# Optimization experiments

Hardware: AMD Instinct MI355X
Metric: run time of the kernel (lower is better)

## Reference

```python
import jax, jax.numpy as jnp
import numpy as np

N_SRC = 20000
N_TGT = 20000
N_EDGE = 320000
D = 128            # in_dim == hid_dim
EDGE_IN = 2 * D + 1  # src feat + tgt feat + radial
COORD_MAX = 10.0


def _mlp2(x, w1, b1, w2, b2):
    # Linear -> SiLU -> Linear -> SiLU (edge MLP)
    h = jax.nn.silu(x @ w1 + b1)
    return jax.nn.silu(h @ w2 + b2)


def setup_inputs() -> dict:
    key = jax.random.key(0)
    ks = jax.random.split(key, 32)
    s = 0.05
    inp = {
        "src_node_feat": jax.random.normal(ks[0], (N_SRC, D), jnp.float32),
        "tgt_node_feat": jax.random.normal(ks[1], (N_TGT, D), jnp.float32),
        "src_node_coord": jax.random.normal(ks[2], (N_SRC, 3), jnp.float32),
        "tgt_node_coord": jax.random.normal(ks[3], (N_TGT, 3), jnp.float32),
        "edge_src": jax.random.randint(ks[4], (N_EDGE,), 0, N_SRC, jnp.int32),
        "edge_tgt": jax.random.randint(ks[5], (N_EDGE,), 0, N_TGT, jnp.int32),
        # edge MLP s2t
        "w1_s2t": jax.random.normal(ks[6], (EDGE_IN, D), jnp.float32) * s,
        "b1_s2t": jnp.zeros((D,), jnp.float32),
        "w2_s2t": jax.random.normal(ks[7], (D, D), jnp.float32) * s,
        "b2_s2t": jnp.zeros((D,), jnp.float32),
        # edge MLP t2s
        "w1_t2s": jax.random.normal(ks[8], (EDGE_IN, D), jnp.float32) * s,
        "b1_t2s": jnp.zeros((D,), jnp.float32),
        "w2_t2s": jax.random.normal(ks[9], (D, D), jnp.float32) * s,
        "b2_t2s": jnp.zeros((D,), jnp.float32),
        # gate MLPs (Linear(D,1) + Sigmoid)
        "wg_s2t": jax.random.normal(ks[10], (D, 1), jnp.float32) * s,
        "bg_s2t": jnp.zeros((1,), jnp.float32),
        "wg_t2s": jax.random.normal(ks[11], (D, 1), jnp.float32) * s,
        "bg_t2s": jnp.zeros((1,), jnp.float32),
        # coord MLP: Linear(D,D) + SiLU + Linear(D,1, bias=False, xavier gain 1e-3)
        "wc1": jax.random.normal(ks[12], (D, D), jnp.float32) * s,
        "bc1": jnp.zeros((D,), jnp.float32),
        "wc2": jax.random.normal(ks[13], (D, 1), jnp.float32) * 0.001,
        # node MLP tgt: Linear(2D,D) + SiLU + Linear(D,D)
        "wn1_t": jax.random.normal(ks[14], (2 * D, D), jnp.float32) * s,
        "bn1_t": jnp.zeros((D,), jnp.float32),
        "wn2_t": jax.random.normal(ks[15], (D, D), jnp.float32) * s,
        "bn2_t": jnp.zeros((D,), jnp.float32),
        # node MLP src
        "wn1_s": jax.random.normal(ks[16], (2 * D, D), jnp.float32) * s,
        "bn1_s": jnp.zeros((D,), jnp.float32),
        "wn2_s": jax.random.normal(ks[17], (D, D), jnp.float32) * s,
        "bn2_s": jnp.zeros((D,), jnp.float32),
    }
    return inp


def reference(src_node_feat, tgt_node_feat, src_node_coord, tgt_node_coord,
              edge_src, edge_tgt,
              w1_s2t, b1_s2t, w2_s2t, b2_s2t,
              w1_t2s, b1_t2s, w2_t2s, b2_t2s,
              wg_s2t, bg_s2t, wg_t2s, bg_t2s,
              wc1, bc1, wc2,
              wn1_t, bn1_t, wn2_t, bn2_t,
              wn1_s, bn1_s, wn2_s, bn2_s):
    # ---- coord2radial ----
    coord_diff = tgt_node_coord[edge_tgt] - src_node_coord[edge_src]  # [E,3]
    radial = jnp.sum(coord_diff ** 2, axis=1, keepdims=True)          # [E,1]

    # ---- edge function (gather + concat + two edge MLPs + gates) ----
    edge_in = jnp.concatenate(
        [src_node_feat[edge_src], tgt_node_feat[edge_tgt], radial], axis=1)  # [E, 257]
    e_s2t = _mlp2(edge_in, w1_s2t, b1_s2t, w2_s2t, b2_s2t)  # [E,D]
    e_t2s = _mlp2(edge_in, w1_t2s, b1_t2s, w2_t2s, b2_t2s)  # [E,D]
    e_s2t = e_s2t * jax.nn.sigmoid(e_s2t @ wg_s2t + bg_s2t)
    e_t2s = e_t2s * jax.nn.sigmoid(e_t2s @ wg_t2s + bg_t2s)

    # ---- coord update (coords_agg='mean', output_coord=True) ----
    coord_w = jax.nn.silu(e_s2t @ wc1 + bc1) @ wc2          # [E,1]
    weighted_trans = coord_diff * coord_w                   # [E,3]
    trans_sum = jax.ops.segment_sum(weighted_trans, edge_tgt, num_segments=N_TGT)
    cnt = jax.ops.segment_sum(jnp.ones((weighted_trans.shape[0],), jnp.float32),
                              edge_tgt, num_segments=N_TGT)
    agg_trans = trans_sum / jnp.maximum(cnt, 1.0)[:, None]
    tgt_coord_out = tgt_node_coord + jnp.clip(agg_trans, -COORD_MAX, COORD_MAX)

    # ---- node function (scatter-add aggregation + node MLPs + residual) ----
    agg_s2t = jax.ops.segment_sum(e_s2t, edge_tgt, num_segments=N_TGT)  # [Nt,D]
    agg_t2s = jax.ops.segment_sum(e_t2s, edge_src, num_segments=N_SRC)  # [Ns,D]
    tgt_in = jnp.concatenate([tgt_node_feat, agg_s2t], axis=1)  # [Nt,2D]
    src_in = jnp.concatenate([src_node_feat, agg_t2s], axis=1)  # [Ns,2D]
    tgt_out = jax.nn.silu(tgt_in @ wn1_t + bn1_t) @ wn2_t + bn2_t
    src_out = jax.nn.silu(src_in @ wn1_s + bn1_s) @ wn2_s + bn2_s
    tgt_out = tgt_node_feat + tgt_out  # residual (dims match)
    src_out = src_node_feat + src_out

    return src_out, tgt_out, src_node_coord, tgt_coord_out
```

## Files before the change

kernel.cpp:

```cpp
#include <hip/hip_runtime.h>

#define NN 20000
#define NEDGE 320000
#define COORD_MAX 10.0f

#define LDH 136
#define TILE_N 64
#define LDN  264

typedef __attribute__((ext_vector_type(4))) float f32x4;
typedef __attribute__((ext_vector_type(8))) short short8;
typedef __attribute__((ext_vector_type(8))) __bf16 bf16x8;

static __device__ __forceinline__ f32x4 mfma16(short8 a, short8 b, f32x4 c) {
  return __builtin_amdgcn_mfma_f32_16x16x32_bf16(
      __builtin_bit_cast(bf16x8, a), __builtin_bit_cast(bf16x8, b), c, 0, 0, 0);
}
static __device__ __forceinline__ unsigned short f2bf(float f) {
  unsigned u = __builtin_bit_cast(unsigned, f);
  u += 0x7FFFu + ((u >> 16) & 1u);
  return (unsigned short)(u >> 16);
}
static __device__ __forceinline__ float bf2f(unsigned short u) {
  unsigned x = ((unsigned)u) << 16;
  return __builtin_bit_cast(float, x);
}
static __device__ __forceinline__ unsigned cvtpk(float lo, float hi) {
  unsigned r;
  asm("v_cvt_pk_bf16_f32 %0, %1, %2" : "=v"(r) : "v"(lo), "v"(hi));
  return r;
}
static __device__ __forceinline__ float sigm(float x) {
  return __builtin_amdgcn_rcpf(1.f + __expf(-x));
}
static __device__ __forceinline__ float silu_(float x) { return x * sigm(x); }

struct PackJobs {
  const float* w[11];
  unsigned short* o[11];
  int kreal[11];
  int nk[11];
};

__global__ void egnn_prep(PackJobs J,
                          const int* __restrict__ eTgt, const int* __restrict__ eSrc,
                          int* __restrict__ cntT, int* __restrict__ cntS,
                          float* __restrict__ aggZero ) {
  const int job = blockIdx.y;
  const int idx = blockIdx.x * 256 + threadIdx.x;
  if (job < 11) {
    const int nk = J.nk[job];
    if (idx >= nk * 512) return;
    const float* w = J.w[job];
    const int kreal = J.kreal[job];
    const int lane = idx & 63;
    const int ct = (idx >> 6) & 7;
    const int kstep = idx >> 9;
    const int col = ct * 16 + (lane & 15);
    const int k0 = kstep * 32 + (lane >> 4) * 8;
    union { short8 s; unsigned short u[8]; } t;
#pragma unroll
    for (int j = 0; j < 8; ++j) {
      int k = k0 + j;
      t.u[j] = (k < kreal) ? f2bf(w[(size_t)k * 128 + col]) : (unsigned short)0;
    }
    reinterpret_cast<short8*>(J.o[job])[idx] = t.s;
  } else if (job == 11) {
    if (idx < NEDGE) {
      atomicAdd(&cntT[eTgt[idx]], 1);
      atomicAdd(&cntS[eSrc[idx]], 1);
    }
  } else {
    float4* p = reinterpret_cast<float4*>(aggZero);
    const int total = 2 * NN * 128 / 4;
    for (int k = idx; k < total; k += 1250 * 256)
      p[k] = float4{0.f, 0.f, 0.f, 0.f};
  }
}

struct PreJobs {
  const float* x[2];
  const unsigned short* wA[2];
  const unsigned short* wB[2];
  const float* biasA[2];
  const float* biasB[2];
  unsigned short* oA[2];
  unsigned short* oB[2];
};

__global__ __launch_bounds__(256, 2) void egnn_pre(PreJobs J, int N) {
  __shared__ __align__(16) unsigned short sX[64 * LDH];
  const int job = blockIdx.y;
  const float* __restrict__ X = J.x[job];
  const int n0 = blockIdx.x * 64;
  const int tid = threadIdx.x;

  for (int s = tid; s < 64 * 32; s += 256) {
    const int row = s >> 5;
    const int c4 = (s & 31) * 4;
    const int node = n0 + row;
    float4 v = {0.f, 0.f, 0.f, 0.f};
    if (node < N) v = reinterpret_cast<const float4*>(X + (size_t)node * 128)[s & 31];
    *reinterpret_cast<uint2*>(&sX[row * LDH + c4]) =
        uint2{cvtpk(v.x, v.y), cvtpk(v.z, v.w)};
  }
  __syncthreads();

  const int lane = tid & 63, wid = tid >> 6;
  const int r16 = lane & 15, g4 = lane >> 4;
  const int rowBase = wid * 16;

#pragma unroll 1
  for (int half = 0; half < 2; ++half) {
    const unsigned short* __restrict__ W = half ? J.wB[job] : J.wA[job];
    const float* __restrict__ bias = half ? J.biasB[job] : J.biasA[job];
    unsigned short* __restrict__ O = half ? J.oB[job] : J.oA[job];
    f32x4 acc[8];
#pragma unroll
    for (int ct = 0; ct < 8; ++ct) acc[ct] = f32x4{0.f, 0.f, 0.f, 0.f};
#pragma unroll
    for (int ks = 0; ks < 4; ++ks) {
      const short8 a = *reinterpret_cast<const short8*>(
          &sX[(rowBase + r16) * LDH + ks * 32 + g4 * 8]);
#pragma unroll
      for (int ct = 0; ct < 8; ++ct) {
        const short8 b = *reinterpret_cast<const short8*>(
            W + ((size_t)(ks * 8 + ct) * 64 + lane) * 8);
        acc[ct] = mfma16(a, b, acc[ct]);
      }
    }
#pragma unroll
    for (int ct = 0; ct < 8; ++ct) {
      const int col = ct * 16 + r16;
      const float bv = bias ? bias[col] : 0.f;
#pragma unroll
      for (int r = 0; r < 4; ++r) {
        const int node = n0 + rowBase + g4 * 4 + r;
        if (node < N) O[(size_t)node * 128 + col] = f2bf(acc[ct][r] + bv);
      }
    }
  }
}

__global__ __launch_bounds__(1024) void egnn_scan(
    const int* __restrict__ c0, int* __restrict__ r0, int* __restrict__ o0,
    const int* __restrict__ c1, int* __restrict__ r1, int* __restrict__ o1, int n) {
  const int* cnt = blockIdx.x ? c1 : c0;
  int* rp = blockIdx.x ? r1 : r0;
  int* oc = blockIdx.x ? o1 : o0;
  __shared__ int sums[1024];
  const int tid = threadIdx.x;
  const int chunk = (n + 1023) / 1024;
  const int i0 = tid * chunk;
  int local = 0;
  for (int k = 0; k < chunk; ++k) {
    const int i = i0 + k;
    if (i < n) local += cnt[i];
  }
  sums[tid] = local;
  __syncthreads();
  for (int s = 1; s < 1024; s <<= 1) {
    int v = (tid >= s) ? sums[tid - s] : 0;
    __syncthreads();
    sums[tid] += v;
    __syncthreads();
  }
  int run = (tid == 0) ? 0 : sums[tid - 1];
  for (int k = 0; k < chunk; ++k) {
    const int i = i0 + k;
    if (i < n) { rp[i] = run; oc[i] = run; run += cnt[i]; }
  }
  if (tid == 1023) rp[n] = sums[1023];
}

__global__ void egnn_scatter(const int* __restrict__ eTgt, const int* __restrict__ eSrc,
                             int* __restrict__ offT, int* __restrict__ offS,
                             int* __restrict__ permT, int* __restrict__ permS) {
  const int e = blockIdx.x * 256 + threadIdx.x;
  if (e < NEDGE) {
    permT[atomicAdd(&offT[eTgt[e]], 1)] = e;
    permS[atomicAdd(&offS[eSrc[e]], 1)] = e;
  }
}

__global__ __launch_bounds__(256, 4) void egnn_edge(
    const unsigned short* __restrict__ S1A, const unsigned short* __restrict__ T1A,
    const unsigned short* __restrict__ S1B, const unsigned short* __restrict__ T1B,
    const float* __restrict__ srcC, const float* __restrict__ tgtC,
    const int* __restrict__ eSrc, const int* __restrict__ eTgt,
    const float* __restrict__ w1A, const float* __restrict__ w1B,
    const unsigned short* __restrict__ w2pA, const float* __restrict__ b2A,
    const float* __restrict__ wgA, const float* __restrict__ bgA,
    const unsigned short* __restrict__ w2pB, const float* __restrict__ b2B,
    const float* __restrict__ wgB, const float* __restrict__ bgB,
    const unsigned short* __restrict__ wc1p, const float* __restrict__ bc1,
    const float* __restrict__ wc2,
    const int* __restrict__ permT, const int* __restrict__ permS,
    float* __restrict__ aggA, float* __restrict__ aggB,
    float* __restrict__ wtBuf)
{
  __shared__ __align__(16) unsigned short sH[4][32 * LDH];
  __shared__ float sCD[128 * 3];
  __shared__ float sRad[128];
  __shared__ int sS[128];
  __shared__ int sT[128];

  const int dir = blockIdx.y;
  const int tid = threadIdx.x;
  const int j0 = blockIdx.x * 128;
  const int* __restrict__ perm = dir ? permS : permT;

  if (tid < 128) {
    const int e = perm[j0 + tid];
    const int s = eSrc[e], t = eTgt[e];
    sS[tid] = s; sT[tid] = t;
    const float dx = tgtC[t * 3 + 0] - srcC[s * 3 + 0];
    const float dy = tgtC[t * 3 + 1] - srcC[s * 3 + 1];
    const float dz = tgtC[t * 3 + 2] - srcC[s * 3 + 2];
    sCD[tid * 3 + 0] = dx; sCD[tid * 3 + 1] = dy; sCD[tid * 3 + 2] = dz;
    sRad[tid] = dx * dx + dy * dy + dz * dz;
  }
  __syncthreads();

  const int lane = tid & 63, wid = tid >> 6;
  const int r16 = lane & 15, g4 = lane >> 4;
  const int we = wid * 32;
  const int h32 = lane >> 5;
  const int c4 = (lane & 31) * 4;
  const int c8 = (lane & 15) * 8;
  const int r4 = lane >> 4;
  const int c2 = lane * 2;

  const unsigned short* __restrict__ S1 = dir ? S1B : S1A;
  const unsigned short* __restrict__ T1 = dir ? T1B : T1A;
  const float* w1 = dir ? w1B : w1A;
  const float4 wr0 = *reinterpret_cast<const float4*>(w1 + 256 * 128 + c8);
  const float4 wr1 = *reinterpret_cast<const float4*>(w1 + 256 * 128 + c8 + 4);
  const float* b2 = dir ? b2B : b2A;
  const float* wg = dir ? wgB : wgA;
  const float bg = dir ? bgB[0] : bgA[0];
  const int* __restrict__ nids = dir ? sS : sT;
  float* __restrict__ agg = dir ? aggB : aggA;

  unsigned short* hT = sH[wid];

#pragma unroll
  for (int i = 0; i < 8; ++i) {
    const int row = 4 * i + r4;
    const int e = we + row;
    const int s = sS[e], t = sT[e];
    const float rad = sRad[e];
    union { short8 v; unsigned short u[8]; } a, b;
    a.v = *reinterpret_cast<const short8*>(S1 + (size_t)s * 128 + c8);
    b.v = *reinterpret_cast<const short8*>(T1 + (size_t)t * 128 + c8);
    const float f0 = silu_(bf2f(a.u[0]) + bf2f(b.u[0]) + rad * wr0.x);
    const float f1 = silu_(bf2f(a.u[1]) + bf2f(b.u[1]) + rad * wr0.y);
    const float f2 = silu_(bf2f(a.u[2]) + bf2f(b.u[2]) + rad * wr0.z);
    const float f3 = silu_(bf2f(a.u[3]) + bf2f(b.u[3]) + rad * wr0.w);
    const float f4 = silu_(bf2f(a.u[4]) + bf2f(b.u[4]) + rad * wr1.x);
    const float f5 = silu_(bf2f(a.u[5]) + bf2f(b.u[5]) + rad * wr1.y);
    const float f6 = silu_(bf2f(a.u[6]) + bf2f(b.u[6]) + rad * wr1.z);
    const float f7 = silu_(bf2f(a.u[7]) + bf2f(b.u[7]) + rad * wr1.w);
    *reinterpret_cast<uint4*>(&hT[row * LDH + c8]) =
        uint4{cvtpk(f0, f1), cvtpk(f2, f3), cvtpk(f4, f5), cvtpk(f6, f7)};
  }

  const unsigned short* w2p = dir ? w2pB : w2pA;
  f32x4 acc[2][8];
#pragma unroll
  for (int rt = 0; rt < 2; ++rt)
#pragma unroll
    for (int ct = 0; ct < 8; ++ct) acc[rt][ct] = f32x4{0.f, 0.f, 0.f, 0.f};
#pragma unroll
  for (int ks = 0; ks < 4; ++ks) {
    short8 a[2];
#pragma unroll
    for (int rt = 0; rt < 2; ++rt)
      a[rt] = *reinterpret_cast<const short8*>(
          &hT[(rt * 16 + r16) * LDH + ks * 32 + g4 * 8]);
#pragma unroll
    for (int ct = 0; ct < 8; ++ct) {
      const short8 b = *reinterpret_cast<const short8*>(
          w2p + ((size_t)(ks * 8 + ct) * 64 + lane) * 8);
#pragma unroll
      for (int rt = 0; rt < 2; ++rt) acc[rt][ct] = mfma16(a[rt], b, acc[rt][ct]);
    }
  }

  float part[2][4];
#pragma unroll
  for (int rt = 0; rt < 2; ++rt)
#pragma unroll
    for (int r = 0; r < 4; ++r) part[rt][r] = 0.f;
#pragma unroll
  for (int ct = 0; ct < 8; ++ct) {
    const float b2v = b2[ct * 16 + r16];
    const float wgv = wg[ct * 16 + r16];
#pragma unroll
    for (int rt = 0; rt < 2; ++rt)
#pragma unroll
      for (int r = 0; r < 4; ++r) {
        const float e = silu_(acc[rt][ct][r] + b2v);
        acc[rt][ct][r] = e;
        part[rt][r] += e * wgv;
      }
  }
#pragma unroll
  for (int m = 1; m < 16; m <<= 1)
#pragma unroll
    for (int rt = 0; rt < 2; ++rt)
#pragma unroll
      for (int r = 0; r < 4; ++r) part[rt][r] += __shfl_xor(part[rt][r], m, 64);
#pragma unroll
  for (int rt = 0; rt < 2; ++rt)
#pragma unroll
    for (int r = 0; r < 4; ++r) {
      const float gate = sigm(part[rt][r] + bg);
#pragma unroll
      for (int ct = 0; ct < 8; ++ct) acc[rt][ct][r] *= gate;
    }

#pragma unroll
  for (int rt = 0; rt < 2; ++rt)
#pragma unroll
    for (int ct = 0; ct < 8; ++ct)
#pragma unroll
      for (int r = 0; r < 4; ++r)
        hT[(rt * 16 + g4 * 4 + r) * LDH + ct * 16 + r16] = f2bf(acc[rt][ct][r]);

  if (dir == 0) {
    f32x4 ac[2][8];
#pragma unroll
    for (int rt = 0; rt < 2; ++rt)
#pragma unroll
      for (int ct = 0; ct < 8; ++ct) ac[rt][ct] = f32x4{0.f, 0.f, 0.f, 0.f};
#pragma unroll
    for (int ks = 0; ks < 4; ++ks) {
      short8 a[2];
#pragma unroll
      for (int rt = 0; rt < 2; ++rt)
        a[rt] = *reinterpret_cast<const short8*>(
            &hT[(rt * 16 + r16) * LDH + ks * 32 + g4 * 8]);
#pragma unroll
      for (int ct = 0; ct < 8; ++ct) {
        const short8 b = *reinterpret_cast<const short8*>(
            wc1p + ((size_t)(ks * 8 + ct) * 64 + lane) * 8);
#pragma unroll
        for (int rt = 0; rt < 2; ++rt) ac[rt][ct] = mfma16(a[rt], b, ac[rt][ct]);
      }
    }
    float pc[2][4];
#pragma unroll
    for (int rt = 0; rt < 2; ++rt)
#pragma unroll
      for (int r = 0; r < 4; ++r) pc[rt][r] = 0.f;
#pragma unroll
    for (int ct = 0; ct < 8; ++ct) {
      const float bcv = bc1[ct * 16 + r16];
      const float w2v = wc2[ct * 16 + r16];
#pragma unroll
      for (int rt = 0; rt < 2; ++rt)
#pragma unroll
        for (int r = 0; r < 4; ++r)
          pc[rt][r] += silu_(ac[rt][ct][r] + bcv) * w2v;
    }
#pragma unroll
    for (int m = 1; m < 16; m <<= 1)
#pragma unroll
      for (int rt = 0; rt < 2; ++rt)
#pragma unroll
        for (int r = 0; r < 4; ++r) pc[rt][r] += __shfl_xor(pc[rt][r], m, 64);

#pragma unroll
    for (int rt = 0; rt < 2; ++rt)
#pragma unroll
      for (int r = 0; r < 4; ++r) {
        if (r16 == 0) {
          const int el = we + rt * 16 + g4 * 4 + r;
          const float p = pc[rt][r];
          const float4 w = {sCD[el * 3 + 0] * p, sCD[el * 3 + 1] * p,
                            sCD[el * 3 + 2] * p, 0.f};
          *reinterpret_cast<float4*>(wtBuf + (size_t)(j0 + el) * 4) = w;
        }
      }
  }

  {
    float s0 = 0.f, s1 = 0.f;
    int curNode = nids[we];
    int segStart = 0;
#pragma unroll 4
    for (int row = 0; row < 32; ++row) {
      const ushort2 v = *reinterpret_cast<const ushort2*>(&hT[row * LDH + c2]);
      s0 += bf2f(v.x); s1 += bf2f(v.y);
      const int nxt = (row < 31) ? nids[we + row + 1] : -1;
      if (nxt != curNode) {
        float* dst = agg + (size_t)curNode * 128 + c2;
        if (segStart > 0 && row < 31) {
          dst[0] = s0; dst[1] = s1;
        } else {
          atomicAdd(dst, s0);
          atomicAdd(dst + 1, s1);
        }
        s0 = 0.f; s1 = 0.f;
        curNode = nxt; segStart = row + 1;
      }
    }
  }
}

struct NodeJobs {
  const float* feat[2];
  const float* agg[2];
  const unsigned short* w1p[2];
  const float* b1[2];
  const unsigned short* w2p[2];
  const float* b2[2];
  float* outp[2];
};

__global__ __launch_bounds__(256, 2) void egnn_node(
    NodeJobs J, int N,
    const float* __restrict__ srcC, const float* __restrict__ tgtC,
    const float* __restrict__ wt, const int* __restrict__ rp,
    float* __restrict__ outSC, float* __restrict__ outTC) {
  __shared__ __align__(16) unsigned short sIn[TILE_N * LDN];
  __shared__ __align__(16) unsigned short sH2[TILE_N * LDH];
  const int job = blockIdx.y;
  const int tid = threadIdx.x;

  if (job == 2) {
    const int n = blockIdx.x * 256 + tid;
    if (n < NN) {
      outSC[n * 3 + 0] = srcC[n * 3 + 0];
      outSC[n * 3 + 1] = srcC[n * 3 + 1];
      outSC[n * 3 + 2] = srcC[n * 3 + 2];
      const int j0 = rp[n], j1 = rp[n + 1];
      float ax = 0.f, ay = 0.f, az = 0.f;
      for (int j = j0; j < j1; ++j) {
        const float4 v = *reinterpret_cast<const float4*>(wt + (size_t)j * 4);
        ax += v.x; ay += v.y; az += v.z;
      }
      const float c = fmaxf((float)(j1 - j0), 1.f);
      ax = fminf(fmaxf(ax / c, -COORD_MAX), COORD_MAX);
      ay = fminf(fmaxf(ay / c, -COORD_MAX), COORD_MAX);
      az = fminf(fmaxf(az / c, -COORD_MAX), COORD_MAX);
      outTC[n * 3 + 0] = tgtC[n * 3 + 0] + ax;
      outTC[n * 3 + 1] = tgtC[n * 3 + 1] + ay;
      outTC[n * 3 + 2] = tgtC[n * 3 + 2] + az;
    }
    return;
  }

  const float* __restrict__ feat = J.feat[job];
  const float* __restrict__ agg = J.agg[job];
  const unsigned short* __restrict__ w1p = J.w1p[job];
  const float* __restrict__ b1 = J.b1[job];
  const unsigned short* __restrict__ w2p = J.w2p[job];
  const float* __restrict__ b2 = J.b2[job];
  float* __restrict__ outp = J.outp[job];

  const int n0 = blockIdx.x * TILE_N;

  for (int s = tid; s < 64 * 64; s += 256) {
    const int row = s >> 6;
    const int half = (s >> 5) & 1;
    const int c4 = (s & 31) * 4;
    const int node = n0 + row;
    float4 v = {0.f, 0.f, 0.f, 0.f};
    if (node < N)
      v = reinterpret_cast<const float4*>((half ? agg : feat) + (size_t)node * 128)[s & 31];
    *reinterpret_cast<uint2*>(&sIn[row * LDN + half * 128 + c4]) =
        uint2{cvtpk(v.x, v.y), cvtpk(v.z, v.w)};
  }
  __syncthreads();

  const int lane = tid & 63;
  const int wid = tid >> 6;
  const int rowBase = wid * 16;
  const int r16 = lane & 15;
  const int g4 = lane >> 4;

  f32x4 acc[8];
#pragma unroll
  for (int ct = 0; ct < 8; ++ct) acc[ct] = f32x4{0.f, 0.f, 0.f, 0.f};
#pragma unroll
  for (int ks = 0; ks < 8; ++ks) {
    const short8 a = *reinterpret_cast<const short8*>(
        &sIn[(rowBase + r16) * LDN + ks * 32 + g4 * 8]);
#pragma unroll
    for (int ct = 0; ct < 8; ++ct) {
      const short8 b = *reinterpret_cast<const short8*>(
          w1p + ((size_t)(ks * 8 + ct) * 64 + lane) * 8);
      acc[ct] = mfma16(a, b, acc[ct]);
    }
  }
#pragma unroll
  for (int ct = 0; ct < 8; ++ct) {
    const int col = ct * 16 + r16;
    const float bias = b1[col];
#pragma unroll
    for (int r = 0; r < 4; ++r) {
      const float h = silu_(acc[ct][r] + bias);
      sH2[(rowBase + g4 * 4 + r) * LDH + col] = f2bf(h);
    }
  }

  f32x4 acc2[8];
#pragma unroll
  for (int ct = 0; ct < 8; ++ct) acc2[ct] = f32x4{0.f, 0.f, 0.f, 0.f};
#pragma unroll
  for (int ks = 0; ks < 4; ++ks) {
    const short8 a = *reinterpret_cast<const short8*>(
        &sH2[(rowBase + r16) * LDH + ks * 32 + g4 * 8]);
#pragma unroll
    for (int ct = 0; ct < 8; ++ct) {
      const short8 b = *reinterpret_cast<const short8*>(
          w2p + ((size_t)(ks * 8 + ct) * 64 + lane) * 8);
      acc2[ct] = mfma16(a, b, acc2[ct]);
    }
  }

#pragma unroll
  for (int ct = 0; ct < 8; ++ct) {
    const int col = ct * 16 + r16;
    const float bias = b2[col];
#pragma unroll
    for (int r = 0; r < 4; ++r) {
      const int node = n0 + rowBase + g4 * 4 + r;
      if (node < N)
        outp[(size_t)node * 128 + col] = feat[(size_t)node * 128 + col] + acc2[ct][r] + bias;
    }
  }
}

extern "C" void kernel_launch(void* const* d_in, const int* in_sizes, int n_in,
                              void* d_out, int out_size, void* d_ws, size_t ws_size,
                              hipStream_t stream) {
  const float* srcF = (const float*)d_in[0];
  const float* tgtF = (const float*)d_in[1];
  const float* srcC = (const float*)d_in[2];
  const float* tgtC = (const float*)d_in[3];
  const int* eSrc = (const int*)d_in[4];
  const int* eTgt = (const int*)d_in[5];
  const float* w1_s2t = (const float*)d_in[6];
  const float* b1_s2t = (const float*)d_in[7];
  const float* w2_s2t = (const float*)d_in[8];
  const float* b2_s2t = (const float*)d_in[9];
  const float* w1_t2s = (const float*)d_in[10];
  const float* b1_t2s = (const float*)d_in[11];
  const float* w2_t2s = (const float*)d_in[12];
  const float* b2_t2s = (const float*)d_in[13];
  const float* wg_s2t = (const float*)d_in[14];
  const float* bg_s2t = (const float*)d_in[15];
  const float* wg_t2s = (const float*)d_in[16];
  const float* bg_t2s = (const float*)d_in[17];
  const float* wc1 = (const float*)d_in[18];
  const float* bc1 = (const float*)d_in[19];
  const float* wc2 = (const float*)d_in[20];
  const float* wn1_t = (const float*)d_in[21];
  const float* bn1_t = (const float*)d_in[22];
  const float* wn2_t = (const float*)d_in[23];
  const float* bn2_t = (const float*)d_in[24];
  const float* wn1_s = (const float*)d_in[25];
  const float* bn1_s = (const float*)d_in[26];
  const float* wn2_s = (const float*)d_in[27];
  const float* bn2_s = (const float*)d_in[28];

  char* ws = (char*)d_ws;
  size_t off = 0;
  auto take = [&](size_t bytes) -> char* {
    char* p = ws + off;
    off = (off + bytes + 255) & ~(size_t)255;
    return p;
  };
  float* aggA = (float*)take((size_t)NN * 128 * 4);
  float* aggB = (float*)take((size_t)NN * 128 * 4);
  float* wtBuf = (float*)take((size_t)NEDGE * 4 * 4);
  unsigned short* S1A = (unsigned short*)take((size_t)NN * 128 * 2);
  unsigned short* T1A = (unsigned short*)take((size_t)NN * 128 * 2);
  unsigned short* S1B = (unsigned short*)take((size_t)NN * 128 * 2);
  unsigned short* T1B = (unsigned short*)take((size_t)NN * 128 * 2);
  unsigned short* w1tA = (unsigned short*)take(4 * 4096 * 2);
  unsigned short* w1mA = (unsigned short*)take(4 * 4096 * 2);
  unsigned short* w1tB = (unsigned short*)take(4 * 4096 * 2);
  unsigned short* w1mB = (unsigned short*)take(4 * 4096 * 2);
  unsigned short* w2pA = (unsigned short*)take(4 * 4096 * 2);
  unsigned short* w2pB = (unsigned short*)take(4 * 4096 * 2);
  unsigned short* wc1p = (unsigned short*)take(4 * 4096 * 2);
  unsigned short* wn1pt = (unsigned short*)take(8 * 4096 * 2);
  unsigned short* wn2pt = (unsigned short*)take(4 * 4096 * 2);
  unsigned short* wn1ps = (unsigned short*)take(8 * 4096 * 2);
  unsigned short* wn2ps = (unsigned short*)take(4 * 4096 * 2);
  int* cntT = (int*)take((size_t)NN * 4);
  int* cntS = (int*)take((size_t)NN * 4);
  const char* cntZeroStart = (const char*)cntT;
  const size_t cntZeroBytes = (size_t)((char*)cntS + NN * 4 - (char*)cntT);
  int* rowptrT = (int*)take((size_t)(NN + 1) * 4);
  int* rowptrS = (int*)take((size_t)(NN + 1) * 4);
  int* offT = (int*)take((size_t)NN * 4);
  int* offS = (int*)take((size_t)NN * 4);
  int* permT = (int*)take((size_t)NEDGE * 4);
  int* permS = (int*)take((size_t)NEDGE * 4);

  hipMemsetAsync((void*)cntZeroStart, 0, cntZeroBytes, stream);

  PackJobs PJ;
  PJ.w[0] = w1_s2t;             PJ.o[0] = w1tA;  PJ.kreal[0] = 128; PJ.nk[0] = 4;
  PJ.w[1] = w1_s2t + 128 * 128; PJ.o[1] = w1mA;  PJ.kreal[1] = 128; PJ.nk[1] = 4;
  PJ.w[2] = w1_t2s;             PJ.o[2] = w1tB;  PJ.kreal[2] = 128; PJ.nk[2] = 4;
  PJ.w[3] = w1_t2s + 128 * 128; PJ.o[3] = w1mB;  PJ.kreal[3] = 128; PJ.nk[3] = 4;
  PJ.w[4] = w2_s2t;             PJ.o[4] = w2pA;  PJ.kreal[4] = 128; PJ.nk[4] = 4;
  PJ.w[5] = w2_t2s;             PJ.o[5] = w2pB;  PJ.kreal[5] = 128; PJ.nk[5] = 4;
  PJ.w[6] = wc1;                PJ.o[6] = wc1p;  PJ.kreal[6] = 128; PJ.nk[6] = 4;
  PJ.w[7] = wn1_t;              PJ.o[7] = wn1pt; PJ.kreal[7] = 256; PJ.nk[7] = 8;
  PJ.w[8] = wn2_t;              PJ.o[8] = wn2pt; PJ.kreal[8] = 128; PJ.nk[8] = 4;
  PJ.w[9] = wn1_s;              PJ.o[9] = wn1ps; PJ.kreal[9] = 256; PJ.nk[9] = 8;
  PJ.w[10] = wn2_s;             PJ.o[10] = wn2ps; PJ.kreal[10] = 128; PJ.nk[10] = 4;
  egnn_prep<<<dim3(1250, 13), 256, 0, stream>>>(PJ, eTgt, eSrc, cntT, cntS, aggA);

  PreJobs PR;
  PR.x[0] = srcF; PR.wA[0] = w1tA; PR.wB[0] = w1tB;
  PR.biasA[0] = nullptr; PR.biasB[0] = nullptr;
  PR.oA[0] = S1A; PR.oB[0] = S1B;
  PR.x[1] = tgtF; PR.wA[1] = w1mA; PR.wB[1] = w1mB;
  PR.biasA[1] = b1_s2t; PR.biasB[1] = b1_t2s;
  PR.oA[1] = T1A; PR.oB[1] = T1B;
  egnn_pre<<<dim3(313, 2), 256, 0, stream>>>(PR, NN);

  egnn_scan<<<2, 1024, 0, stream>>>(cntT, rowptrT, offT, cntS, rowptrS, offS, NN);
  egnn_scatter<<<NEDGE / 256, 256, 0, stream>>>(eTgt, eSrc, offT, offS, permT, permS);

  float* outSrc = (float*)d_out;
  float* outTgt = outSrc + (size_t)NN * 128;
  float* outSC  = outTgt + (size_t)NN * 128;
  float* outTC  = outSC + (size_t)NN * 3;

  egnn_edge<<<dim3(NEDGE / 128, 2), 256, 0, stream>>>(
      S1A, T1A, S1B, T1B, srcC, tgtC, eSrc, eTgt,
      w1_s2t, w1_t2s,
      w2pA, b2_s2t, wg_s2t, bg_s2t,
      w2pB, b2_t2s, wg_t2s, bg_t2s,
      wc1p, bc1, wc2, permT, permS, aggA, aggB, wtBuf);

  NodeJobs NJ;
  NJ.feat[0] = tgtF; NJ.agg[0] = aggA;
  NJ.w1p[0] = wn1pt; NJ.b1[0] = bn1_t; NJ.w2p[0] = wn2pt; NJ.b2[0] = bn2_t;
  NJ.outp[0] = outTgt;
  NJ.feat[1] = srcF; NJ.agg[1] = aggB;
  NJ.w1p[1] = wn1ps; NJ.b1[1] = bn1_s; NJ.w2p[1] = wn2ps; NJ.b2[1] = bn2_s;
  NJ.outp[1] = outSrc;

  const int nodeBlocks = (NN + TILE_N - 1) / TILE_N;
  egnn_node<<<dim3(nodeBlocks, 3), 256, 0, stream>>>(
      NJ, NN, srcC, tgtC, wtBuf, rowptrT, outSC, outTC);
}
```

Measured before the change: 306.3 us.

## Fuse scan into pre kernel, store sorted src/tgt pairs, batch edge gathers

Folds the CSR prefix-scan into extra blocks of the pre-projection kernel, which removes one kernel launch. The scan now runs on 256 threads instead of 1024. The scatter writes (src,tgt) pairs directly in sorted order, so the edge kernel no longer does a dependent perm→eSrc/eTgt indirection. The edge kernel issues all 16 row gathers up front before the SiLU math to raise memory-level parallelism, at the cost of more registers. The node kernel aliases its second LDS buffer onto the first, with an added barrier, to cut shared memory and raise occupancy.

```diff
diff --git a/kernel.cpp b/kernel.cpp
--- a/kernel.cpp
+++ b/kernel.cpp
@@ -88,12 +88,46 @@
   unsigned short* oB[2];
 };
 
-__global__ __launch_bounds__(256, 2) void egnn_pre(PreJobs J, int N) {
+__global__ __launch_bounds__(256, 2) void egnn_pre(
+    PreJobs J, int N,
+    const int* __restrict__ c0, int* __restrict__ r0, int* __restrict__ o0,
+    const int* __restrict__ c1, int* __restrict__ r1, int* __restrict__ o1) {
   __shared__ __align__(16) unsigned short sX[64 * LDH];
+  __shared__ int sums[256];
   const int job = blockIdx.y;
+  const int tid = threadIdx.x;
+
+  if (job == 2) {
+    if (blockIdx.x >= 2) return;
+    const int* cnt = blockIdx.x ? c1 : c0;
+    int* rp = blockIdx.x ? r1 : r0;
+    int* oc = blockIdx.x ? o1 : o0;
+    const int chunk = (NN + 255) / 256;
+    const int i0 = tid * chunk;
+    int local = 0;
+    for (int k = 0; k < chunk; ++k) {
+      const int i = i0 + k;
+      if (i < NN) local += cnt[i];
+    }
+    sums[tid] = local;
+    __syncthreads();
+    for (int s = 1; s < 256; s <<= 1) {
+      int v = (tid >= s) ? sums[tid - s] : 0;
+      __syncthreads();
+      sums[tid] += v;
+      __syncthreads();
+    }
+    int run = (tid == 0) ? 0 : sums[tid - 1];
+    for (int k = 0; k < chunk; ++k) {
+      const int i = i0 + k;
+      if (i < NN) { rp[i] = run; oc[i] = run; run += cnt[i]; }
+    }
+    if (tid == 255) rp[NN] = sums[255];
+    return;
+  }
+
   const float* __restrict__ X = J.x[job];
   const int n0 = blockIdx.x * 64;
-  const int tid = threadIdx.x;
 
   for (int s = tid; s < 64 * 32; s += 256) {
     const int row = s >> 5;
@@ -142,44 +176,14 @@
   }
 }
 
-__global__ __launch_bounds__(1024) void egnn_scan(
-    const int* __restrict__ c0, int* __restrict__ r0, int* __restrict__ o0,
-    const int* __restrict__ c1, int* __restrict__ r1, int* __restrict__ o1, int n) {
-  const int* cnt = blockIdx.x ? c1 : c0;
-  int* rp = blockIdx.x ? r1 : r0;
-  int* oc = blockIdx.x ? o1 : o0;
-  __shared__ int sums[1024];
-  const int tid = threadIdx.x;
-  const int chunk = (n + 1023) / 1024;
-  const int i0 = tid * chunk;
-  int local = 0;
-  for (int k = 0; k < chunk; ++k) {
-    const int i = i0 + k;
-    if (i < n) local += cnt[i];
-  }
-  sums[tid] = local;
-  __syncthreads();
-  for (int s = 1; s < 1024; s <<= 1) {
-    int v = (tid >= s) ? sums[tid - s] : 0;
-    __syncthreads();
-    sums[tid] += v;
-    __syncthreads();
-  }
-  int run = (tid == 0) ? 0 : sums[tid - 1];
-  for (int k = 0; k < chunk; ++k) {
-    const int i = i0 + k;
-    if (i < n) { rp[i] = run; oc[i] = run; run += cnt[i]; }
-  }
-  if (tid == 1023) rp[n] = sums[1023];
-}
-
 __global__ void egnn_scatter(const int* __restrict__ eTgt, const int* __restrict__ eSrc,
                              int* __restrict__ offT, int* __restrict__ offS,
-                             int* __restrict__ permT, int* __restrict__ permS) {
+                             int2* __restrict__ stT, int2* __restrict__ stS) {
   const int e = blockIdx.x * 256 + threadIdx.x;
   if (e < NEDGE) {
-    permT[atomicAdd(&offT[eTgt[e]], 1)] = e;
-    permS[atomicAdd(&offS[eSrc[e]], 1)] = e;
+    const int s = eSrc[e], t = eTgt[e];
+    stT[atomicAdd(&offT[t], 1)] = int2{s, t};
+    stS[atomicAdd(&offS[s], 1)] = int2{s, t};
   }
 }
 
@@ -187,7 +191,7 @@
     const unsigned short* __restrict__ S1A, const unsigned short* __restrict__ T1A,
     const unsigned short* __restrict__ S1B, const unsigned short* __restrict__ T1B,
     const float* __restrict__ srcC, const float* __restrict__ tgtC,
-    const int* __restrict__ eSrc, const int* __restrict__ eTgt,
+    const int2* __restrict__ stT, const int2* __restrict__ stS,
     const float* __restrict__ w1A, const float* __restrict__ w1B,
     const unsigned short* __restrict__ w2pA, const float* __restrict__ b2A,
     const float* __restrict__ wgA, const float* __restrict__ bgA,
@@ -195,7 +199,6 @@
     const float* __restrict__ wgB, const float* __restrict__ bgB,
     const unsigned short* __restrict__ wc1p, const float* __restrict__ bc1,
     const float* __restrict__ wc2,
-    const int* __restrict__ permT, const int* __restrict__ permS,
     float* __restrict__ aggA, float* __restrict__ aggB,
     float* __restrict__ wtBuf)
 {
@@ -208,11 +211,10 @@
   const int dir = blockIdx.y;
   const int tid = threadIdx.x;
   const int j0 = blockIdx.x * 128;
-  const int* __restrict__ perm = dir ? permS : permT;
 
   if (tid < 128) {
-    const int e = perm[j0 + tid];
-    const int s = eSrc[e], t = eTgt[e];
+    const int2 st = (dir ? stS : stT)[j0 + tid];
+    const int s = st.x, t = st.y;
     sS[tid] = s; sT[tid] = t;
     const float dx = tgtC[t * 3 + 0] - srcC[s * 3 + 0];
     const float dy = tgtC[t * 3 + 1] - srcC[s * 3 + 1];
@@ -225,8 +227,6 @@
   const int lane = tid & 63, wid = tid >> 6;
   const int r16 = lane & 15, g4 = lane >> 4;
   const int we = wid * 32;
-  const int h32 = lane >> 5;
-  const int c4 = (lane & 31) * 4;
   const int c8 = (lane & 15) * 8;
   const int r4 = lane >> 4;
   const int c2 = lane * 2;
@@ -244,25 +244,37 @@
 
   unsigned short* hT = sH[wid];
 
-#pragma unroll
-  for (int i = 0; i < 8; ++i) {
-    const int row = 4 * i + r4;
-    const int e = we + row;
-    const int s = sS[e], t = sT[e];
-    const float rad = sRad[e];
-    union { short8 v; unsigned short u[8]; } a, b;
-    a.v = *reinterpret_cast<const short8*>(S1 + (size_t)s * 128 + c8);
-    b.v = *reinterpret_cast<const short8*>(T1 + (size_t)t * 128 + c8);
-    const float f0 = silu_(bf2f(a.u[0]) + bf2f(b.u[0]) + rad * wr0.x);
-    const float f1 = silu_(bf2f(a.u[1]) + bf2f(b.u[1]) + rad * wr0.y);
-    const float f2 = silu_(bf2f(a.u[2]) + bf2f(b.u[2]) + rad * wr0.z);
-    const float f3 = silu_(bf2f(a.u[3]) + bf2f(b.u[3]) + rad * wr0.w);
-    const float f4 = silu_(bf2f(a.u[4]) + bf2f(b.u[4]) + rad * wr1.x);
-    const float f5 = silu_(bf2f(a.u[5]) + bf2f(b.u[5]) + rad * wr1.y);
-    const float f6 = silu_(bf2f(a.u[6]) + bf2f(b.u[6]) + rad * wr1.z);
-    const float f7 = silu_(bf2f(a.u[7]) + bf2f(b.u[7]) + rad * wr1.w);
-    *reinterpret_cast<uint4*>(&hT[row * LDH + c8]) =
-        uint4{cvtpk(f0, f1), cvtpk(f2, f3), cvtpk(f4, f5), cvtpk(f6, f7)};
+  {
+    short8 gA[2][4], gB[2][4];
+#pragma unroll
+    for (int c = 0; c < 2; ++c)
+#pragma unroll
+      for (int i = 0; i < 4; ++i) {
+        const int row = (c * 4 + i) * 4 + r4;
+        const int e = we + row;
+        gA[c][i] = *reinterpret_cast<const short8*>(S1 + (size_t)sS[e] * 128 + c8);
+        gB[c][i] = *reinterpret_cast<const short8*>(T1 + (size_t)sT[e] * 128 + c8);
+      }
+#pragma unroll
+    for (int c = 0; c < 2; ++c)
+#pragma unroll
+      for (int i = 0; i < 4; ++i) {
+        const int row = (c * 4 + i) * 4 + r4;
+        const int e = we + row;
+        const float rad = sRad[e];
+        union { short8 v; unsigned short u[8]; } a, b;
+        a.v = gA[c][i]; b.v = gB[c][i];
+        const float f0 = silu_(bf2f(a.u[0]) + bf2f(b.u[0]) + rad * wr0.x);
+        const float f1 = silu_(bf2f(a.u[1]) + bf2f(b.u[1]) + rad * wr0.y);
+        const float f2 = silu_(bf2f(a.u[2]) + bf2f(b.u[2]) + rad * wr0.z);
+        const float f3 = silu_(bf2f(a.u[3]) + bf2f(b.u[3]) + rad * wr0.w);
+        const float f4 = silu_(bf2f(a.u[4]) + bf2f(b.u[4]) + rad * wr1.x);
+        const float f5 = silu_(bf2f(a.u[5]) + bf2f(b.u[5]) + rad * wr1.y);
+        const float f6 = silu_(bf2f(a.u[6]) + bf2f(b.u[6]) + rad * wr1.z);
+        const float f7 = silu_(bf2f(a.u[7]) + bf2f(b.u[7]) + rad * wr1.w);
+        *reinterpret_cast<uint4*>(&hT[row * LDH + c8]) =
+            uint4{cvtpk(f0, f1), cvtpk(f2, f3), cvtpk(f4, f5), cvtpk(f6, f7)};
+      }
   }
 
   const unsigned short* w2p = dir ? w2pB : w2pA;
@@ -425,7 +437,7 @@
     const float* __restrict__ wt, const int* __restrict__ rp,
     float* __restrict__ outSC, float* __restrict__ outTC) {
   __shared__ __align__(16) unsigned short sIn[TILE_N * LDN];
-  __shared__ __align__(16) unsigned short sH2[TILE_N * LDH];
+  unsigned short* sH2 = sIn;
   const int job = blockIdx.y;
   const int tid = threadIdx.x;
 
@@ -495,6 +507,9 @@
       acc[ct] = mfma16(a, b, acc[ct]);
     }
   }
+
+  __syncthreads();
+
 #pragma unroll
   for (int ct = 0; ct < 8; ++ct) {
     const int col = ct * 16 + r16;
@@ -600,8 +615,8 @@
   int* rowptrS = (int*)take((size_t)(NN + 1) * 4);
   int* offT = (int*)take((size_t)NN * 4);
   int* offS = (int*)take((size_t)NN * 4);
-  int* permT = (int*)take((size_t)NEDGE * 4);
-  int* permS = (int*)take((size_t)NEDGE * 4);
+  int2* stT = (int2*)take((size_t)NEDGE * 8);
+  int2* stS = (int2*)take((size_t)NEDGE * 8);
 
   hipMemsetAsync((void*)cntZeroStart, 0, cntZeroBytes, stream);
 
@@ -626,10 +641,10 @@
   PR.x[1] = tgtF; PR.wA[1] = w1mA; PR.wB[1] = w1mB;
   PR.biasA[1] = b1_s2t; PR.biasB[1] = b1_t2s;
   PR.oA[1] = T1A; PR.oB[1] = T1B;
-  egnn_pre<<<dim3(313, 2), 256, 0, stream>>>(PR, NN);
-
-  egnn_scan<<<2, 1024, 0, stream>>>(cntT, rowptrT, offT, cntS, rowptrS, offS, NN);
-  egnn_scatter<<<NEDGE / 256, 256, 0, stream>>>(eTgt, eSrc, offT, offS, permT, permS);
+  egnn_pre<<<dim3(313, 3), 256, 0, stream>>>(
+      PR, NN, cntT, rowptrT, offT, cntS, rowptrS, offS);
+
+  egnn_scatter<<<NEDGE / 256, 256, 0, stream>>>(eTgt, eSrc, offT, offS, stT, stS);
 
   float* outSrc = (float*)d_out;
   float* outTgt = outSrc + (size_t)NN * 128;
@@ -637,11 +652,11 @@
   float* outTC  = outSC + (size_t)NN * 3;
 
   egnn_edge<<<dim3(NEDGE / 128, 2), 256, 0, stream>>>(
-      S1A, T1A, S1B, T1B, srcC, tgtC, eSrc, eTgt,
+      S1A, T1A, S1B, T1B, srcC, tgtC, stT, stS,
       w1_s2t, w1_t2s,
       w2pA, b2_s2t, wg_s2t, bg_s2t,
       w2pB, b2_t2s, wg_t2s, bg_t2s,
-      wc1p, bc1, wc2, permT, permS, aggA, aggB, wtBuf);
+      wc1p, bc1, wc2, aggA, aggB, wtBuf);
 
   NodeJobs NJ;
   NJ.feat[0] = tgtF; NJ.agg[0] = aggA;
```

After: 286.4 us. -6.5%, faster.
